# Kernel optimization log

Hardware: AMD Instinct MI355X
Metric: run time of the kernel (lower is better)

## Reference

```python
import jax, jax.numpy as jnp
import numpy as np

DIM = 512
CODEBOOK_SIZE = 8192
B, N = 8, 2048
EPS = 1e-12


def setup_inputs() -> dict:
    key = jax.random.key(0)
    k1, k2, k3 = jax.random.split(key, 3)
    x = jax.random.normal(k1, (B, N, DIM), dtype=jnp.float32)
    # matches torch.randn(codebook_size, dim) * dim ** -0.5
    codebook = jax.random.normal(k2, (CODEBOOK_SIZE, DIM), dtype=jnp.float32) * DIM ** -0.5
    # nn.Linear(dim, dim, bias=False) weight, applied as x @ W.T
    W = jax.random.normal(k3, (DIM, DIM), dtype=jnp.float32) * DIM ** -0.5
    return {"x": x, "codebook": codebook, "W": W}


def _l2norm(t):
    return t / jnp.maximum(jnp.linalg.norm(t, axis=-1, keepdims=True), EPS)


def _rotate_from_to(q, x):
    """Rotation trick: forward value == q, gradient flows through x via a
    detached Householder-style rotation (R = I - 2ww^T + 2 q_hat x_hat^T)
    and detached norm rescaling."""
    sg = jax.lax.stop_gradient
    norm_x = jnp.linalg.norm(x, axis=-1, keepdims=True)
    norm_q = jnp.linalg.norm(q, axis=-1, keepdims=True)
    x_hat = x / jnp.maximum(norm_x, EPS)
    q_hat = q / jnp.maximum(norm_q, EPS)
    w = sg(_l2norm(x_hat + q_hat))
    x_hat_d, q_hat_d = sg(x_hat), sg(q_hat)
    e = x
    rotated = (e
               - 2.0 * jnp.sum(e * w, axis=-1, keepdims=True) * w
               + 2.0 * jnp.sum(e * x_hat_d, axis=-1, keepdims=True) * q_hat_d)
    return rotated * sg(norm_q / jnp.maximum(norm_x, EPS))


def reference(x, codebook, W):
    # implicit codebook = Linear(codebook)
    codes = jnp.einsum('cd,ed->ce', codebook, W)  # [C, d]
    d2 = -2.0 * jnp.einsum('bnd,cd->bnc', x, codes) + jnp.sum(codes * codes, axis=-1)
    indices = jnp.argmin(jax.lax.stop_gradient(d2), axis=-1)  # [b, n] int
    quantized = codes[indices]  # gather -> [b, n, d]
    commit_loss = jnp.mean((jax.lax.stop_gradient(x) - quantized) ** 2)
    quantized = _rotate_from_to(quantized, x)
    return quantized, indices, commit_loss
```

## Files before the change

kernel.cpp:

```cpp
#include <hip/hip_runtime.h>


#define DIMK  512
#define CBN   8192
#define MROWS 16384

#define SX 24.0f
#define SC 500.0f
#define INV_SS (1.0f / (SX * SC))
#define DKEY  1231
#define NSLOT 3

#define WS_CODES   0UL
#define WS_XQ      16777216UL
#define WS_CQ      25165824UL
#define WS_NORMS   29360128UL
#define WS_CAND    29392896UL
#define WS_CBH     29392896UL
#define WS_CBL     37781504UL
#define WS_WH      54558720UL
#define WS_WL      55083008UL
#define WS_LOSSP   55607296UL

typedef short s16x8 __attribute__((ext_vector_type(8)));
typedef int   i32x4 __attribute__((ext_vector_type(4)));
typedef float f32x4 __attribute__((ext_vector_type(4)));

__device__ __forceinline__ unsigned short f2bf(float f) {
    unsigned u = __float_as_uint(f);
    unsigned r = u + 0x7FFFu + ((u >> 16) & 1u);
    return (unsigned short)(r >> 16);
}
__device__ __forceinline__ float bf2f(unsigned short h) {
    return __uint_as_float(((unsigned)h) << 16);
}
__device__ __forceinline__ void load_lds16(const void* g, void* l) {
    __builtin_amdgcn_global_load_lds((const __attribute__((address_space(1))) void*)g,
                                     (__attribute__((address_space(3))) void*)l,
                                     16, 0, 0);
}
__device__ __forceinline__ signed char q8(float v, float s) {
    return (signed char)__float2int_rn(fminf(fmaxf(v * s, -127.0f), 127.0f));
}

__global__ __launch_bounds__(256) void prep(
        const float* __restrict__ x, const float* __restrict__ cb, const float* __restrict__ W,
        signed char* __restrict__ xq,
        unsigned short* __restrict__ cbh, unsigned short* __restrict__ cbl,
        unsigned short* __restrict__ wh, unsigned short* __restrict__ wl,
        float* __restrict__ norms) {
    const int b = blockIdx.x;
    const int t = threadIdx.x;
    if (b < 8192) {
        const int i = b * 256 + t;
        float4 v = ((const float4*)x)[i];
        char4 c;
        c.x = q8(v.x, SX); c.y = q8(v.y, SX); c.z = q8(v.z, SX); c.w = q8(v.w, SX);
        ((char4*)xq)[i] = c;
    } else if (b < 12288) {
        const int i = (b - 8192) * 256 + t;
        float4 v = ((const float4*)cb)[i];
        ushort4 h, l;
        h.x = f2bf(v.x); l.x = f2bf(v.x - bf2f(h.x));
        h.y = f2bf(v.y); l.y = f2bf(v.y - bf2f(h.y));
        h.z = f2bf(v.z); l.z = f2bf(v.z - bf2f(h.z));
        h.w = f2bf(v.w); l.w = f2bf(v.w - bf2f(h.w));
        ((ushort4*)cbh)[i] = h;
        ((ushort4*)cbl)[i] = l;
    } else if (b < 12544) {
        const int i = (b - 12288) * 256 + t;
        float4 v = ((const float4*)W)[i];
        ushort4 h, l;
        h.x = f2bf(v.x); l.x = f2bf(v.x - bf2f(h.x));
        h.y = f2bf(v.y); l.y = f2bf(v.y - bf2f(h.y));
        h.z = f2bf(v.z); l.z = f2bf(v.z - bf2f(h.z));
        h.w = f2bf(v.w); l.w = f2bf(v.w - bf2f(h.w));
        ((ushort4*)wh)[i] = h;
        ((ushort4*)wl)[i] = l;
    } else {
        const int i = (b - 12544) * 256 + t;
        norms[i] = 0.0f;
    }
}

__global__ __launch_bounds__(256) void codes_mfma(
        const unsigned short* __restrict__ Ah_g, const unsigned short* __restrict__ Al_g,
        const unsigned short* __restrict__ Bh_g, const unsigned short* __restrict__ Bl_g,
        float* __restrict__ C, signed char* __restrict__ Cq, float* __restrict__ Norms) {
    __shared__ __align__(16) unsigned short Ahi[2][128 * 32];
    __shared__ __align__(16) unsigned short Alo[2][128 * 32];
    __shared__ __align__(16) unsigned short Bhi[2][128 * 32];
    __shared__ __align__(16) unsigned short Blo[2][128 * 32];

    const int t    = threadIdx.x;
    const int w    = t >> 6;
    const int lane = t & 63;
    const int quad = lane >> 4;
    const int l16  = lane & 15;
    const int wm   = w & 1, wn = w >> 1;
    const int rowBase = blockIdx.x * 128;
    const int colBase = blockIdx.y * 128;

    f32x4 acc[4][4];
    #pragma unroll
    for (int i = 0; i < 4; ++i)
        #pragma unroll
        for (int j = 0; j < 4; ++j)
            acc[i][j] = (f32x4)(0.0f);

    const int mr = t >> 2;
    const int kq = ((t & 3) ^ ((t >> 3) & 3)) * 8;
    const size_t gxa = (size_t)(rowBase + mr) * DIMK + kq;
    const size_t gxb = gxa + (size_t)64 * DIMK;
    const size_t gca = (size_t)(colBase + mr) * DIMK + kq;
    const size_t gcb = gca + (size_t)64 * DIMK;
    const int l0 = w * 512;
    const int l1 = 2048 + w * 512;

    const int swz8 = (quad ^ ((l16 >> 1) & 3)) * 8;

#define CODES_STAGE(NXT, K0)                                   \
    do {                                                       \
        load_lds16(Ah_g + gxa + (K0), &Ahi[NXT][l0]);          \
        load_lds16(Ah_g + gxb + (K0), &Ahi[NXT][l1]);          \
        load_lds16(Al_g + gxa + (K0), &Alo[NXT][l0]);          \
        load_lds16(Al_g + gxb + (K0), &Alo[NXT][l1]);          \
        load_lds16(Bh_g + gca + (K0), &Bhi[NXT][l0]);          \
        load_lds16(Bh_g + gcb + (K0), &Bhi[NXT][l1]);          \
        load_lds16(Bl_g + gca + (K0), &Blo[NXT][l0]);          \
        load_lds16(Bl_g + gcb + (K0), &Blo[NXT][l1]);          \
    } while (0)

#define CODES_COMPUTE(CUR)                                                                         \
    do {                                                                                           \
        s16x8 ah[4], al[4], bh[4], bl[4];                                                          \
        _Pragma("unroll")                                                                          \
        for (int i = 0; i < 4; ++i) {                                                              \
            const int m = wm * 64 + i * 16 + l16;                                                  \
            ah[i] = *(const s16x8*)&Ahi[CUR][m * 32 + swz8];                                       \
            al[i] = *(const s16x8*)&Alo[CUR][m * 32 + swz8];                                       \
        }                                                                                          \
        _Pragma("unroll")                                                                          \
        for (int j = 0; j < 4; ++j) {                                                              \
            const int n = wn * 64 + j * 16 + l16;                                                  \
            bh[j] = *(const s16x8*)&Bhi[CUR][n * 32 + swz8];                                       \
            bl[j] = *(const s16x8*)&Blo[CUR][n * 32 + swz8];                                       \
        }                                                                                          \
        _Pragma("unroll")                                                                          \
        for (int i = 0; i < 4; ++i)                                                                \
            _Pragma("unroll")                                                                      \
            for (int j = 0; j < 4; ++j) {                                                          \
                acc[i][j] = __builtin_amdgcn_mfma_f32_16x16x32_bf16(ah[i], bh[j], acc[i][j], 0, 0, 0); \
                acc[i][j] = __builtin_amdgcn_mfma_f32_16x16x32_bf16(ah[i], bl[j], acc[i][j], 0, 0, 0); \
                acc[i][j] = __builtin_amdgcn_mfma_f32_16x16x32_bf16(al[i], bh[j], acc[i][j], 0, 0, 0); \
            }                                                                                      \
    } while (0)

    CODES_STAGE(0, 0);
    asm volatile("s_waitcnt vmcnt(0)" ::: "memory");
    __syncthreads();

    for (int k0 = 0; k0 < DIMK; k0 += 64) {
        CODES_STAGE(1, k0 + 32);
        CODES_COMPUTE(0);
        asm volatile("s_waitcnt vmcnt(0)" ::: "memory");
        __syncthreads();
        if (k0 + 64 < DIMK) {
            CODES_STAGE(0, k0 + 64);
            CODES_COMPUTE(1);
            asm volatile("s_waitcnt vmcnt(0)" ::: "memory");
            __syncthreads();
        } else {
            CODES_COMPUTE(1);
        }
    }
#undef CODES_STAGE
#undef CODES_COMPUTE

    #pragma unroll
    for (int i = 0; i < 4; ++i) {
        #pragma unroll
        for (int r = 0; r < 4; ++r) {
            const int row = rowBase + wm * 64 + i * 16 + quad * 4 + r;
            float nsum = 0.0f;
            #pragma unroll
            for (int j = 0; j < 4; ++j) {
                const int col = colBase + wn * 64 + j * 16 + l16;
                const float v = acc[i][j][r];
                C[(size_t)row * DIMK + col] = v;
                Cq[(size_t)row * DIMK + col] = q8(v, SC);
                nsum = fmaf(v, v, nsum);
            }
            nsum += __shfl_xor(nsum, 1, 64);
            nsum += __shfl_xor(nsum, 2, 64);
            nsum += __shfl_xor(nsum, 4, 64);
            nsum += __shfl_xor(nsum, 8, 64);
            if (l16 == 0) atomicAdd(&Norms[row], nsum);
        }
    }
}

__global__ __launch_bounds__(512, 6) void d2_argmin_i8(
        const signed char* __restrict__ Xq,
        const signed char* __restrict__ Cq,
        const float* __restrict__ Norms,
        unsigned* __restrict__ Cand) {
    __shared__ __align__(16) signed char Ash[2][128 * 64];
    __shared__ __align__(16) signed char Bsh[2][128 * 64];

    const int t    = threadIdx.x;
    const int w    = t >> 6;
    const int lane = t & 63;
    const int quad = lane >> 4;
    const int l16  = lane & 15;
    const int wm   = w & 3, wn = w >> 2;
    const int rowBase = blockIdx.x * 128;
    const int colBase = blockIdx.y * 128;

    i32x4 acc[2][4];
    #pragma unroll
    for (int i = 0; i < 2; ++i)
        #pragma unroll
        for (int j = 0; j < 4; ++j)
            acc[i][j] = (i32x4)(0);

    const int mr  = t >> 2;
    const int kcs = ((t & 3) ^ ((t >> 3) & 3)) * 16;
    const size_t gxa = (size_t)(rowBase + mr) * DIMK + kcs;
    const size_t gca = (size_t)(colBase + mr) * DIMK + kcs;
    const int lb = w * 1024;

    const int swz  = (quad ^ ((l16 >> 1) & 3)) * 16;
    const int aoff = (wm * 32 + l16) * 64 + swz;
    const int boff = (wn * 64 + l16) * 64 + swz;

    float nq[4];
    #pragma unroll
    for (int j = 0; j < 4; ++j)
        nq[j] = fmaf(Norms[colBase + wn * 64 + j * 16 + l16], 4096.0f, 65536.0f);

#define D2_STEP(CUR, NXT, K0, DO_STAGE, DO_SYNC)                                                   \
    do {                                                                                           \
        if (DO_STAGE) {                                                                            \
            load_lds16(Xq + gxa + (K0) + 64, &Ash[NXT][lb]);                                       \
            load_lds16(Cq + gca + (K0) + 64, &Bsh[NXT][lb]);                                       \
        }                                                                                          \
        i32x4 af0 = *(const i32x4*)&Ash[CUR][aoff];                                                \
        i32x4 af1 = *(const i32x4*)&Ash[CUR][aoff + 1024];                                         \
        _Pragma("unroll")                                                                          \
        for (int j = 0; j < 4; ++j) {                                                              \
            const i32x4 bfj = *(const i32x4*)&Bsh[CUR][boff + j * 1024];                           \
            acc[0][j] = __builtin_amdgcn_mfma_i32_16x16x64_i8(af0, bfj, acc[0][j], 0, 0, 0);       \
            acc[1][j] = __builtin_amdgcn_mfma_i32_16x16x64_i8(af1, bfj, acc[1][j], 0, 0, 0);       \
        }                                                                                          \
        if (DO_SYNC) {                                                                             \
            asm volatile("s_waitcnt vmcnt(0)" ::: "memory");                                       \
            __syncthreads();                                                                       \
        }                                                                                          \
    } while (0)

    load_lds16(Xq + gxa, &Ash[0][lb]);
    load_lds16(Cq + gca, &Bsh[0][lb]);
    asm volatile("s_waitcnt vmcnt(0)" ::: "memory");
    __syncthreads();

    D2_STEP(0, 1,   0, true,  true);
    D2_STEP(1, 0,  64, true,  true);
    D2_STEP(0, 1, 128, true,  true);
    D2_STEP(1, 0, 192, true,  true);
    D2_STEP(0, 1, 256, true,  true);
    D2_STEP(1, 0, 320, true,  true);
    D2_STEP(0, 1, 384, true,  true);
    D2_STEP(1, 0, 448, false, false);
#undef D2_STEP

    const unsigned colG = colBase + wn * 64 + l16;
    const int subtile = blockIdx.y * 2 + wn;
    const float C2 = -8192.0f * INV_SS;

    #pragma unroll
    for (int i = 0; i < 2; ++i) {
        #pragma unroll
        for (int r = 0; r < 4; ++r) {
            unsigned k[4];
            #pragma unroll
            for (int j = 0; j < 4; ++j) {
                const float kf = fmaf((float)acc[i][j][r], C2, nq[j]);
                int ki = (int)kf;
                ki = ki < 0 ? 0 : ki;
                ki = ki > 524287 ? 524287 : ki;
                k[j] = ((unsigned)ki << 13) | (colG + j * 16);
            }
            unsigned lo01 = min(k[0], k[1]), hi01 = max(k[0], k[1]);
            unsigned lo23 = min(k[2], k[3]), hi23 = max(k[2], k[3]);
            unsigned a0 = min(lo01, lo23);
            unsigned m  = max(lo01, lo23);
            unsigned tt = min(hi01, hi23);
            unsigned a1 = min(m, tt);
            unsigned a2 = max(m, tt);
            #pragma unroll
            for (int mk = 1; mk < 16; mk <<= 1) {
                const unsigned b0 = __shfl_xor(a0, mk, 64);
                const unsigned b1 = __shfl_xor(a1, mk, 64);
                const unsigned b2 = __shfl_xor(a2, mk, 64);
                const unsigned M0 = max(a0, b0);
                const unsigned m1 = min(a1, b1);
                const unsigned n0 = min(a0, b0);
                a2 = min(max(m1, M0), min(a2, b2));
                a1 = min(M0, m1);
                a0 = n0;
            }
            if (l16 == 0) {
                const int row = rowBase + wm * 32 + i * 16 + quad * 4 + r;
                unsigned* slot = Cand + ((size_t)row * 128 + subtile) * NSLOT;
                slot[0] = a0; slot[1] = a1; slot[2] = a2;
            }
        }
    }
}

__global__ __launch_bounds__(256) void refine_gather(
        const float* __restrict__ X, const float* __restrict__ Codes,
        const float* __restrict__ Norms, const unsigned* __restrict__ Cand,
        float* __restrict__ outQ, float* __restrict__ outIdx,
        float* __restrict__ lossP) {
    const int t    = threadIdx.x;
    const int w    = t >> 6;
    const int lane = t & 63;
    const int row  = blockIdx.x * 4 + w;

    const unsigned* cp = Cand + (size_t)row * 128 * NSLOT + lane * 6;
    unsigned sl[6];
    #pragma unroll
    for (int s = 0; s < 6; ++s) sl[s] = cp[s];

    unsigned mn = sl[0];
    #pragma unroll
    for (int s = 1; s < 6; ++s) mn = min(mn, sl[s]);
    #pragma unroll
    for (int mask = 1; mask < 64; mask <<= 1)
        mn = min(mn, (unsigned)__shfl((int)mn, lane ^ mask, 64));
    const unsigned thrp = (((mn >> 13) + DKEY) << 13) | 0x1FFFu;

    const float4 xa = *(const float4*)(X + (size_t)row * DIMK + lane * 8);
    const float4 xb = *(const float4*)(X + (size_t)row * DIMK + lane * 8 + 4);

    float bestD = __builtin_inff();
    unsigned bestIdx = 0xFFFFFFFFu;

    #pragma unroll
    for (int s = 0; s < 6; ++s) {
        unsigned long long bm = __ballot(sl[s] <= thrp);
        while (bm) {
            const int src = __ffsll(bm) - 1;
            bm &= bm - 1;
            const unsigned sv = (unsigned)__shfl((int)sl[s], src, 64);
            const unsigned idx = sv & 0x1FFFu;
            const float4 ca = *(const float4*)(Codes + (size_t)idx * DIMK + lane * 8);
            const float4 cbv = *(const float4*)(Codes + (size_t)idx * DIMK + lane * 8 + 4);
            float s2 = xa.x * ca.x + xa.y * ca.y + xa.z * ca.z + xa.w * ca.w
                     + xb.x * cbv.x + xb.y * cbv.y + xb.z * cbv.z + xb.w * cbv.w;
            #pragma unroll
            for (int mm = 1; mm < 64; mm <<= 1) s2 += __shfl_xor(s2, mm, 64);
            const float d2 = fmaf(-2.0f, s2, Norms[idx]);
            if (d2 < bestD || (d2 == bestD && idx < bestIdx)) { bestD = d2; bestIdx = idx; }
        }
    }

    const float4 qa = *(const float4*)(Codes + (size_t)bestIdx * DIMK + lane * 8);
    const float4 qb = *(const float4*)(Codes + (size_t)bestIdx * DIMK + lane * 8 + 4);
    *(float4*)(outQ + (size_t)row * DIMK + lane * 8) = qa;
    *(float4*)(outQ + (size_t)row * DIMK + lane * 8 + 4) = qb;
    float dx0 = xa.x - qa.x, dx1 = xa.y - qa.y, dx2 = xa.z - qa.z, dx3 = xa.w - qa.w;
    float dy0 = xb.x - qb.x, dy1 = xb.y - qb.y, dy2 = xb.z - qb.z, dy3 = xb.w - qb.w;
    float s = dx0 * dx0 + dx1 * dx1 + dx2 * dx2 + dx3 * dx3
            + dy0 * dy0 + dy1 * dy1 + dy2 * dy2 + dy3 * dy3;
    #pragma unroll
    for (int off = 32; off > 0; off >>= 1) s += __shfl_down(s, off);
    if (lane == 0) {
        lossP[row] = s;
        outIdx[row] = (float)bestIdx;
    }
}

__global__ __launch_bounds__(256) void finalize_loss(const float* __restrict__ lossPartials,
                                                     float* __restrict__ outLoss) {
    const int t = threadIdx.x;
    float s = 0.0f;
    for (int i = t; i < MROWS; i += 256) s += lossPartials[i];
    #pragma unroll
    for (int off = 32; off > 0; off >>= 1) s += __shfl_down(s, off);
    __shared__ float red[4];
    if ((t & 63) == 0) red[t >> 6] = s;
    __syncthreads();
    if (t == 0)
        *outLoss = (red[0] + red[1] + red[2] + red[3]) * (1.0f / (float)((size_t)MROWS * DIMK));
}

extern "C" void kernel_launch(void* const* d_in, const int* in_sizes, int n_in,
                              void* d_out, int out_size, void* d_ws, size_t ws_size,
                              hipStream_t stream) {
    const float* x  = (const float*)d_in[0];
    const float* cb = (const float*)d_in[1];
    const float* W  = (const float*)d_in[2];
    float* out = (float*)d_out;

    char* ws = (char*)d_ws;
    float* codes          = (float*)(ws + WS_CODES);
    signed char* xq       = (signed char*)(ws + WS_XQ);
    signed char* cq       = (signed char*)(ws + WS_CQ);
    float* norms          = (float*)(ws + WS_NORMS);
    unsigned* cand        = (unsigned*)(ws + WS_CAND);
    unsigned short* cbh   = (unsigned short*)(ws + WS_CBH);
    unsigned short* cbl   = (unsigned short*)(ws + WS_CBL);
    unsigned short* wh    = (unsigned short*)(ws + WS_WH);
    unsigned short* wl    = (unsigned short*)(ws + WS_WL);
    float* lossP          = (float*)(ws + WS_LOSSP);

    prep<<<12576, 256, 0, stream>>>(x, cb, W, xq, cbh, cbl, wh, wl, norms);

    codes_mfma<<<dim3(CBN / 128, DIMK / 128), 256, 0, stream>>>(cbh, cbl, wh, wl, codes, cq, norms);

    d2_argmin_i8<<<dim3(MROWS / 128, CBN / 128), 512, 0, stream>>>(xq, cq, norms, cand);

    refine_gather<<<MROWS / 4, 256, 0, stream>>>(x, codes, norms, cand, out,
                                                 out + (size_t)MROWS * DIMK, lossP);
    finalize_loss<<<1, 256, 0, stream>>>(lossP, out + (size_t)MROWS * DIMK + MROWS);
}
```

Before: 292.7 us.

## Use 8 waves in codes GEMM and refine four candidates per wave concurrently

The codes GEMM block grows from 4 to 8 waves, each owning a 32x64 sub-tile, so each thread issues half as many LDS staging loads and holds fewer accumulators. The refine kernel splits each wave into four 16-lane groups that score four candidate codes at once, using a shorter 4-step reduction, then merges the per-group best with a cross-lane argmin. The aim is more latency hiding in the small GEMM and fewer serial shuffle-reduction rounds per candidate. The cost is more registers for the x row cached per lane and an extra final reduction pass.

```diff
diff --git a/kernel.cpp b/kernel.cpp
--- a/kernel.cpp
+++ b/kernel.cpp
@@ -83,7 +83,7 @@
     }
 }
 
-__global__ __launch_bounds__(256) void codes_mfma(
+__global__ __launch_bounds__(512) void codes_mfma(
         const unsigned short* __restrict__ Ah_g, const unsigned short* __restrict__ Al_g,
         const unsigned short* __restrict__ Bh_g, const unsigned short* __restrict__ Bl_g,
         float* __restrict__ C, signed char* __restrict__ Cq, float* __restrict__ Norms) {
@@ -97,13 +97,13 @@
     const int lane = t & 63;
     const int quad = lane >> 4;
     const int l16  = lane & 15;
-    const int wm   = w & 1, wn = w >> 1;
+    const int wm   = w & 3, wn = w >> 2;
     const int rowBase = blockIdx.x * 128;
     const int colBase = blockIdx.y * 128;
 
-    f32x4 acc[4][4];
-    #pragma unroll
-    for (int i = 0; i < 4; ++i)
+    f32x4 acc[2][4];
+    #pragma unroll
+    for (int i = 0; i < 2; ++i)
         #pragma unroll
         for (int j = 0; j < 4; ++j)
             acc[i][j] = (f32x4)(0.0f);
@@ -111,32 +111,25 @@
     const int mr = t >> 2;
     const int kq = ((t & 3) ^ ((t >> 3) & 3)) * 8;
     const size_t gxa = (size_t)(rowBase + mr) * DIMK + kq;
-    const size_t gxb = gxa + (size_t)64 * DIMK;
     const size_t gca = (size_t)(colBase + mr) * DIMK + kq;
-    const size_t gcb = gca + (size_t)64 * DIMK;
     const int l0 = w * 512;
-    const int l1 = 2048 + w * 512;
 
     const int swz8 = (quad ^ ((l16 >> 1) & 3)) * 8;
 
 #define CODES_STAGE(NXT, K0)                                   \
     do {                                                       \
         load_lds16(Ah_g + gxa + (K0), &Ahi[NXT][l0]);          \
-        load_lds16(Ah_g + gxb + (K0), &Ahi[NXT][l1]);          \
         load_lds16(Al_g + gxa + (K0), &Alo[NXT][l0]);          \
-        load_lds16(Al_g + gxb + (K0), &Alo[NXT][l1]);          \
         load_lds16(Bh_g + gca + (K0), &Bhi[NXT][l0]);          \
-        load_lds16(Bh_g + gcb + (K0), &Bhi[NXT][l1]);          \
         load_lds16(Bl_g + gca + (K0), &Blo[NXT][l0]);          \
-        load_lds16(Bl_g + gcb + (K0), &Blo[NXT][l1]);          \
     } while (0)
 
 #define CODES_COMPUTE(CUR)                                                                         \
     do {                                                                                           \
-        s16x8 ah[4], al[4], bh[4], bl[4];                                                          \
+        s16x8 ah[2], al[2], bh[4], bl[4];                                                          \
         _Pragma("unroll")                                                                          \
-        for (int i = 0; i < 4; ++i) {                                                              \
-            const int m = wm * 64 + i * 16 + l16;                                                  \
+        for (int i = 0; i < 2; ++i) {                                                              \
+            const int m = wm * 32 + i * 16 + l16;                                                  \
             ah[i] = *(const s16x8*)&Ahi[CUR][m * 32 + swz8];                                       \
             al[i] = *(const s16x8*)&Alo[CUR][m * 32 + swz8];                                       \
         }                                                                                          \
@@ -147,7 +140,7 @@
             bl[j] = *(const s16x8*)&Blo[CUR][n * 32 + swz8];                                       \
         }                                                                                          \
         _Pragma("unroll")                                                                          \
-        for (int i = 0; i < 4; ++i)                                                                \
+        for (int i = 0; i < 2; ++i)                                                                \
             _Pragma("unroll")                                                                      \
             for (int j = 0; j < 4; ++j) {                                                          \
                 acc[i][j] = __builtin_amdgcn_mfma_f32_16x16x32_bf16(ah[i], bh[j], acc[i][j], 0, 0, 0); \
@@ -178,10 +171,10 @@
 #undef CODES_COMPUTE
 
     #pragma unroll
-    for (int i = 0; i < 4; ++i) {
+    for (int i = 0; i < 2; ++i) {
         #pragma unroll
         for (int r = 0; r < 4; ++r) {
-            const int row = rowBase + wm * 64 + i * 16 + quad * 4 + r;
+            const int row = rowBase + wm * 32 + i * 16 + quad * 4 + r;
             float nsum = 0.0f;
             #pragma unroll
             for (int j = 0; j < 4; ++j) {
@@ -327,6 +320,8 @@
     const int t    = threadIdx.x;
     const int w    = t >> 6;
     const int lane = t & 63;
+    const int quad = lane >> 4;
+    const int l16  = lane & 15;
     const int row  = blockIdx.x * 4 + w;
 
     const unsigned* cp = Cand + (size_t)row * 128 * NSLOT + lane * 6;
@@ -342,8 +337,10 @@
         mn = min(mn, (unsigned)__shfl((int)mn, lane ^ mask, 64));
     const unsigned thrp = (((mn >> 13) + DKEY) << 13) | 0x1FFFu;
 
-    const float4 xa = *(const float4*)(X + (size_t)row * DIMK + lane * 8);
-    const float4 xb = *(const float4*)(X + (size_t)row * DIMK + lane * 8 + 4);
+    float4 xr[8];
+    #pragma unroll
+    for (int u = 0; u < 8; ++u)
+        xr[u] = *(const float4*)(X + (size_t)row * DIMK + l16 * 32 + u * 4);
 
     float bestD = __builtin_inff();
     unsigned bestIdx = 0xFFFFFFFFu;
@@ -352,21 +349,42 @@
     for (int s = 0; s < 6; ++s) {
         unsigned long long bm = __ballot(sl[s] <= thrp);
         while (bm) {
-            const int src = __ffsll(bm) - 1;
-            bm &= bm - 1;
+            unsigned long long mq = bm;
+            if (quad >= 1) mq &= mq - 1;
+            if (quad >= 2) mq &= mq - 1;
+            if (quad >= 3) mq &= mq - 1;
+            const bool act = (mq != 0ull);
+            const int src = act ? (__ffsll((long long)mq) - 1) : 0;
             const unsigned sv = (unsigned)__shfl((int)sl[s], src, 64);
             const unsigned idx = sv & 0x1FFFu;
-            const float4 ca = *(const float4*)(Codes + (size_t)idx * DIMK + lane * 8);
-            const float4 cbv = *(const float4*)(Codes + (size_t)idx * DIMK + lane * 8 + 4);
-            float s2 = xa.x * ca.x + xa.y * ca.y + xa.z * ca.z + xa.w * ca.w
-                     + xb.x * cbv.x + xb.y * cbv.y + xb.z * cbv.z + xb.w * cbv.w;
+            const float* cr = Codes + (size_t)idx * DIMK + l16 * 32;
+            float s2 = 0.0f;
             #pragma unroll
-            for (int mm = 1; mm < 64; mm <<= 1) s2 += __shfl_xor(s2, mm, 64);
+            for (int u = 0; u < 8; ++u) {
+                const float4 cv = *(const float4*)(cr + u * 4);
+                s2 += xr[u].x * cv.x + xr[u].y * cv.y + xr[u].z * cv.z + xr[u].w * cv.w;
+            }
+            s2 += __shfl_xor(s2, 1, 64);
+            s2 += __shfl_xor(s2, 2, 64);
+            s2 += __shfl_xor(s2, 4, 64);
+            s2 += __shfl_xor(s2, 8, 64);
             const float d2 = fmaf(-2.0f, s2, Norms[idx]);
-            if (d2 < bestD || (d2 == bestD && idx < bestIdx)) { bestD = d2; bestIdx = idx; }
+            if (act && (d2 < bestD || (d2 == bestD && idx < bestIdx))) {
+                bestD = d2; bestIdx = idx;
+            }
+            bm &= bm - 1; bm &= bm - 1; bm &= bm - 1; bm &= bm - 1;
         }
     }
 
+    #pragma unroll
+    for (int mk = 1; mk < 64; mk <<= 1) {
+        const float od = __shfl_xor(bestD, mk, 64);
+        const unsigned oi = (unsigned)__shfl_xor((int)bestIdx, mk, 64);
+        if (od < bestD || (od == bestD && oi < bestIdx)) { bestD = od; bestIdx = oi; }
+    }
+
+    const float4 xa = *(const float4*)(X + (size_t)row * DIMK + lane * 8);
+    const float4 xb = *(const float4*)(X + (size_t)row * DIMK + lane * 8 + 4);
     const float4 qa = *(const float4*)(Codes + (size_t)bestIdx * DIMK + lane * 8);
     const float4 qb = *(const float4*)(Codes + (size_t)bestIdx * DIMK + lane * 8 + 4);
     *(float4*)(outQ + (size_t)row * DIMK + lane * 8) = qa;
@@ -419,7 +437,7 @@
 
     prep<<<12576, 256, 0, stream>>>(x, cb, W, xq, cbh, cbl, wh, wl, norms);
 
-    codes_mfma<<<dim3(CBN / 128, DIMK / 128), 256, 0, stream>>>(cbh, cbl, wh, wl, codes, cq, norms);
+    codes_mfma<<<dim3(CBN / 128, DIMK / 128), 512, 0, stream>>>(cbh, cbl, wh, wl, codes, cq, norms);
 
     d2_argmin_i8<<<dim3(MROWS / 128, CBN / 128), 512, 0, stream>>>(xq, cq, norms, cand);
 
```

Measured after the change: 310.0 us. +5.9%, slower.
